# Kernel optimization log

Hardware: AMD Instinct MI355X
Metric: run time of the kernel (lower is better)

## Reference

```python
import jax, jax.numpy as jnp
import numpy as np

SDIM, VDIM, HID, DEPTH = 128, 3, 64, 4
N, E = 50000, 800000
CUTOFF = 5.0


def setup_inputs() -> dict:
    key = jax.random.key(0)
    ks = jax.random.split(key, 16)
    s = jax.random.normal(ks[0], (N, SDIM), jnp.float32)
    v = jax.random.normal(ks[1], (N, 3, VDIM), jnp.float32)
    edge_index = jax.random.randint(ks[2], (2, E), 0, N, dtype=jnp.int32).astype(jnp.int64)
    d = jax.random.uniform(ks[3], (E,), jnp.float32) * CUTOFF
    r = jax.random.normal(ks[4], (E, 3), jnp.float32)
    r = r / jnp.linalg.norm(r, axis=-1, keepdims=True)
    batch = jnp.zeros((N,), jnp.int64)

    def w(k, shape):
        return jax.random.normal(k, shape, jnp.float32) / jnp.sqrt(jnp.float32(shape[-2]))

    return {
        's': s, 'v': v, 'edge_index': edge_index, 'd': d, 'r': r, 'batch': batch,
        'We1': w(ks[5], (DEPTH, 2 * SDIM + 1, HID)), 'be1': jnp.zeros((DEPTH, HID), jnp.float32),
        'We2': w(ks[6], (DEPTH, HID, HID)), 'be2': jnp.zeros((DEPTH, HID), jnp.float32),
        'Wn1': w(ks[7], (DEPTH, SDIM + HID, HID)), 'bn1': jnp.zeros((DEPTH, HID), jnp.float32),
        'Wn2': w(ks[8], (DEPTH, HID, SDIM)), 'bn2': jnp.zeros((DEPTH, SDIM), jnp.float32),
        'Wv': w(ks[9], (DEPTH, HID, 2 * VDIM)), 'bv': jnp.zeros((DEPTH, 2 * VDIM), jnp.float32),
    }


def _egcl(s, v, src, dst, d, r, C, deg, We1, be1, We2, be2, Wn1, bn1, Wn2, bn2, Wv, bv):
    n = s.shape[0]
    # edge message MLP on gathered endpoint features + distance
    x = jnp.concatenate([s[dst], s[src], d[:, None]], axis=-1)   # [E, 2*SDIM+1]
    h = jax.nn.silu(x @ We1 + be1)
    h = jax.nn.silu(h @ We2 + be2)
    h = h * C[:, None]                                            # cutoff envelope
    # scalar update
    agg_s = jax.ops.segment_sum(h, dst, num_segments=n)           # [N, HID]
    u = jax.nn.silu(jnp.concatenate([s, agg_s], axis=-1) @ Wn1 + bn1)
    s = s + (u @ Wn2 + bn2)
    # equivariant vector update: gated neighbor vectors + gated edge directions
    gates = h @ Wv + bv                                           # [E, 2*VDIM]
    g1, g2 = gates[:, :VDIM], gates[:, VDIM:]
    mv = v[src] * g1[:, None, :] + r[:, :, None] * g2[:, None, :] # [E, 3, VDIM]
    agg_v = jax.ops.segment_sum(mv, dst, num_segments=n) / deg[:, None, None]  # mean aggr
    v = v + agg_v
    return s, v


def reference(s, v, edge_index, d, r, batch, We1, be1, We2, be2, Wn1, bn1, Wn2, bn2, Wv, bv):
    src, dst = edge_index[0], edge_index[1]
    C = 0.5 * (jnp.cos(jnp.pi * d / CUTOFF) + 1.0) * (d < CUTOFF).astype(d.dtype)
    deg = jax.ops.segment_sum(jnp.ones_like(d), dst, num_segments=s.shape[0])
    deg = jnp.maximum(deg, 1.0)
    for i in range(DEPTH):
        s, v = _egcl(s, v, src, dst, d, r, C, deg,
                     We1[i], be1[i], We2[i], be2[i],
                     Wn1[i], bn1[i], Wn2[i], bn2[i], Wv[i], bv[i])
    return (s, v)
```

## Files before the change

### kernel.cpp

```cpp
#include <hip/hip_runtime.h>
#include <math.h>

#define SDIM 128
#define HID 64
#define DEPTH 4
#define CUTOFF_F 5.0f
#define CHUNK 4096

typedef __attribute__((ext_vector_type(8))) short bf16x8;
typedef __attribute__((ext_vector_type(4))) float f32x4;
typedef float4 __attribute__((aligned(4))) float4_u;

__device__ __forceinline__ float silu_f(float x) {
    float e = __expf(-x);
    return x * __builtin_amdgcn_rcpf(1.0f + e);
}

__device__ __forceinline__ unsigned short f2bf(float x) {
    __bf16 b = (__bf16)x;
    return __builtin_bit_cast(unsigned short, b);
}
__device__ __forceinline__ unsigned int f2bf2(float a, float b) {
    return (unsigned int)f2bf(a) | ((unsigned int)f2bf(b) << 16);
}
__device__ __forceinline__ float bf2f(unsigned short u) {
    return __uint_as_float(((unsigned int)u) << 16);
}

struct f8 { float v[8]; };
__device__ __forceinline__ f8 load8(const float* p) {
    f8 r;
    float4 a = *(const float4*)p;
    float4 b = *(const float4*)(p + 4);
    r.v[0]=a.x; r.v[1]=a.y; r.v[2]=a.z; r.v[3]=a.w;
    r.v[4]=b.x; r.v[5]=b.y; r.v[6]=b.z; r.v[7]=b.w;
    return r;
}
__device__ __forceinline__ bf16x8 pack8(const float* h) {
    bf16x8 o;
#pragma unroll
    for (int j = 0; j < 8; ++j) o[j] = (short)f2bf(h[j]);
    return o;
}
__device__ __forceinline__ void unpack8(bf16x8 b, float* o) {
#pragma unroll
    for (int j = 0; j < 8; ++j)
        o[j] = __uint_as_float(((unsigned int)(unsigned short)b[j]) << 16);
}

__global__ void detect_idx_kernel(const void* ei, int N, int* flag) {
    int lane = threadIdx.x;
    const long long* p64 = (const long long*)ei;
    long long v = p64[lane];
    bool ok = (v >= 0 && v < (long long)N);
    unsigned long long m = __ballot(ok);
    if (lane == 0) *flag = (m == ~0ull) ? 1 : 0;
}

__global__ void decode_idx_kernel(const void* ei, int E, int N, const int* flag,
                                  int* __restrict__ srcw, int* __restrict__ dstw,
                                  int* __restrict__ deg_i) {
    int i = blockIdx.x * blockDim.x + threadIdx.x;
    if (i >= 2 * E) return;
    int v;
    if (*flag) v = (int)((const long long*)ei)[i];
    else       v = ((const int*)ei)[i];
    v = min(max(v, 0), N - 1);
    if (i < E) {
        srcw[i] = v;
    } else {
        dstw[i - E] = v;
        atomicAdd(&deg_i[v], 1);
    }
}

__global__ __launch_bounds__(256) void scan1_kernel(const int* __restrict__ deg_i,
                                                    int* __restrict__ part, int N) {
    __shared__ int wsum[4];
    int b = blockIdx.x, t = threadIdx.x;
    int base = b * CHUNK;
    int sum = 0;
    for (int i = t; i < CHUNK; i += 256) {
        int idx = base + i;
        sum += (idx < N) ? deg_i[idx] : 0;
    }
#pragma unroll
    for (int off = 32; off; off >>= 1) sum += __shfl_down(sum, off, 64);
    if ((t & 63) == 0) wsum[t >> 6] = sum;
    __syncthreads();
    if (t == 0) part[b] = wsum[0] + wsum[1] + wsum[2] + wsum[3];
}

__global__ void scan2_kernel(int* __restrict__ part, int* __restrict__ row_start,
                             int B1, int N) {
    int t = threadIdx.x;
    int v = (t < B1) ? part[t] : 0;
    int incl = v;
#pragma unroll
    for (int off = 1; off < 64; off <<= 1) {
        int x = __shfl_up(incl, off, 64);
        if (t >= off) incl += x;
    }
    if (t < B1) part[t] = incl - v;
    if (t == 63) row_start[N] = incl;
}

__global__ __launch_bounds__(256) void scan3_kernel(const int* __restrict__ deg_i,
                                                    const int* __restrict__ part,
                                                    int* __restrict__ row_start, int N) {
    __shared__ int wsum[4];
    __shared__ int carry_s;
    int b = blockIdx.x, t = threadIdx.x;
    int lane = t & 63, w = t >> 6;
    if (t == 0) carry_s = part[b];
    __syncthreads();
    int base0 = b * CHUNK;
    for (int base = base0; base < base0 + CHUNK; base += 256) {
        int i = base + t;
        int v = (i < N) ? deg_i[i] : 0;
        int incl = v;
#pragma unroll
        for (int off = 1; off < 64; off <<= 1) {
            int x = __shfl_up(incl, off, 64);
            if (lane >= off) incl += x;
        }
        if (lane == 63) wsum[w] = incl;
        __syncthreads();
        int wpre = 0;
#pragma unroll
        for (int k = 0; k < 4; ++k) if (k < w) wpre += wsum[k];
        int total = wsum[0] + wsum[1] + wsum[2] + wsum[3];
        int carry = carry_s;
        if (i < N) row_start[i] = carry + wpre + incl - v;
        __syncthreads();
        if (t == 0) carry_s = carry + total;
        __syncthreads();
    }
}

__global__ void scatter_kernel(const int* __restrict__ srcw, const int* __restrict__ dstw,
                               const float* __restrict__ dvec, const float* __restrict__ rvec,
                               const int* __restrict__ row_start, int* __restrict__ cursor,
                               float* __restrict__ rec, int E) {
    int e = blockIdx.x * blockDim.x + threadIdx.x;
    if (e >= E) return;
    int dd = dstw[e];
    int ofs = atomicAdd(&cursor[dd], 1);
    int pos = row_start[dd] + ofs;
    float dv = dvec[e];
    float c = 0.5f * (cosf(3.14159265358979323846f * dv * (1.0f / CUTOFF_F)) + 1.0f);
    c = (dv < CUTOFF_F) ? c : 0.0f;
    float4 r0 = make_float4(__int_as_float(srcw[e]), __int_as_float(dd), dv, c);
    float4 r1 = make_float4(rvec[(size_t)e * 3 + 0], rvec[(size_t)e * 3 + 1],
                            rvec[(size_t)e * 3 + 2], 0.0f);
    *(float4*)(rec + (size_t)pos * 8)     = r0;
    *(float4*)(rec + (size_t)pos * 8 + 4) = r1;
}

__global__ __launch_bounds__(256) void wprep_kernel(
    const float* __restrict__ We1, const float* __restrict__ We2,
    const float* __restrict__ Wv,  const float* __restrict__ Wn1,
    const float* __restrict__ Wn2,
    unsigned short* __restrict__ We1t, unsigned short* __restrict__ We2t,
    unsigned short* __restrict__ Wvt,  unsigned short* __restrict__ Wn1t,
    unsigned short* __restrict__ Wn2t) {
    int l = blockIdx.x, t = threadIdx.x;
    const float* W2 = We2 + (size_t)l * HID * HID;
    unsigned short* T2 = We2t + (size_t)l * HID * HID;
    for (int idx = t; idx < HID * HID; idx += 256) {
        int n = idx >> 6, k = idx & 63;
        T2[n * 64 + k] = f2bf(W2[k * HID + n]);
    }
    const float* Wvl = Wv + (size_t)l * HID * 6;
    unsigned short* Tv = Wvt + (size_t)l * 16 * 64;
    for (int idx = t; idx < 16 * 64; idx += 256) {
        int n = idx >> 6, k = idx & 63;
        Tv[idx] = (n < 6) ? f2bf(Wvl[k * 6 + n]) : (unsigned short)0;
    }
    const float* W1 = We1 + (size_t)l * 257 * 64;
    unsigned short* T1 = We1t + (size_t)l * 128 * 128;
    for (int idx = t; idx < 128 * 128; idx += 256) {
        int n = idx >> 7, k = idx & 127;
        float w = (n < 64) ? W1[(size_t)k * 64 + n] : W1[(size_t)(k + 128) * 64 + (n - 64)];
        T1[n * 128 + k] = f2bf(w);
    }
    const float* Wn1l = Wn1 + (size_t)l * 192 * 64;
    unsigned short* Tn1 = Wn1t + (size_t)l * 64 * 192;
    for (int idx = t; idx < 64 * 192; idx += 256) {
        int n = idx / 192, k = idx - n * 192;
        Tn1[idx] = f2bf(Wn1l[(size_t)k * 64 + n]);
    }
    const float* Wn2l = Wn2 + (size_t)l * 64 * 128;
    unsigned short* Tn2 = Wn2t + (size_t)l * 128 * 64;
    for (int idx = t; idx < 128 * 64; idx += 256) {
        int n = idx >> 6, k = idx & 63;
        Tn2[idx] = f2bf(Wn2l[(size_t)k * 128 + n]);
    }
}

__global__ __launch_bounds__(128) void node_pre_kernel(
    const float* __restrict__ s, const unsigned short* __restrict__ We1t,
    const float* __restrict__ be1,
    unsigned short* __restrict__ Pa, unsigned short* __restrict__ Pb, int N)
{
    __shared__ unsigned short sa[16 * 136];
    int t = threadIdx.x;
    int lane = t & 63, w = t >> 6;
    int n0 = blockIdx.x * 16;
    for (int idx = t; idx < 512; idx += 128) {
        int rl = idx >> 5, c4 = (idx & 31) << 2;
        int n = n0 + rl;
        float4 val = make_float4(0.f, 0.f, 0.f, 0.f);
        if (n < N) val = *(const float4*)(s + (size_t)n * SDIM + c4);
        *(uint2*)(sa + rl * 136 + c4) = make_uint2(f2bf2(val.x, val.y), f2bf2(val.z, val.w));
    }
    __syncthreads();
    int lm = lane & 15, lq = lane >> 4;
    int nr = n0 + lm;
    bool rowok = (nr < N);

    bf16x8 af[4];
#pragma unroll
    for (int kc = 0; kc < 4; ++kc)
        af[kc] = *(const bf16x8*)(sa + lm * 136 + kc * 32 + lq * 8);

#pragma unroll
    for (int ct2 = 0; ct2 < 4; ++ct2) {
        int ct = w * 4 + ct2;
        f32x4 acc = {0.f, 0.f, 0.f, 0.f};
#pragma unroll
        for (int kc = 0; kc < 4; ++kc) {
            bf16x8 b = *(const bf16x8*)(We1t + (size_t)(ct * 16 + lm) * 128 + kc * 32 + lq * 8);
            acc = __builtin_amdgcn_mfma_f32_16x16x32_bf16(b, af[kc], acc, 0, 0, 0);
        }
        if (rowok) {
            if (ct < 4) {
                float4 b4 = *(const float4*)(be1 + ct * 16 + lq * 4);
                *(uint2*)(Pa + (size_t)nr * HID + ct * 16 + lq * 4) =
                    make_uint2(f2bf2(acc[0] + b4.x, acc[1] + b4.y),
                               f2bf2(acc[2] + b4.z, acc[3] + b4.w));
            } else {
                *(uint2*)(Pb + (size_t)nr * HID + (ct - 4) * 16 + lq * 4) =
                    make_uint2(f2bf2(acc[0], acc[1]), f2bf2(acc[2], acc[3]));
            }
        }
    }
}

__global__ __launch_bounds__(256) void edge_kernel(
    const float* __restrict__ rec,
    const unsigned short* __restrict__ Pa, const unsigned short* __restrict__ Pb,
    const float* __restrict__ wd,
    const unsigned short* __restrict__ We2t, const float* __restrict__ be2,
    const unsigned short* __restrict__ Wvt, const float* __restrict__ bv,
    const float* __restrict__ v,
    float* __restrict__ agg_s, float* __restrict__ agg_v, int E)
{
    __shared__ unsigned short hb[64 * 72];
    __shared__ float  gl[64 * 8];
    __shared__ float  vb[64 * 12];
    __shared__ int    m_dst[64];
    __shared__ float4 m_r4[64];
    int t = threadIdx.x;
    int e0 = blockIdx.x * 64;
    int lane = t & 63, w = t >> 6;
    int lm = lane & 15, lq = lane >> 4;
    int m0 = w * 16, rm = m0 + lm;
    int ka = lq * 8, kb = 32 + lq * 8;

    int e  = e0 + rm;
    int ec = min(e, E - 1);
    float4 r0 = *(const float4*)(rec + (size_t)ec * 8);
    int srcr = __float_as_int(r0.x);
    int dstr = __float_as_int(r0.y);
    float dv = r0.z;
    float Cr = (e < E) ? r0.w : 0.0f;

    const unsigned short* pa = Pa + (size_t)dstr * HID;
    const unsigned short* pb = Pb + (size_t)srcr * HID;
    bf16x8 ba0 = *(const bf16x8*)(pa + ka);
    bf16x8 bb0 = *(const bf16x8*)(pb + ka);
    bf16x8 ba1 = *(const bf16x8*)(pa + kb);
    bf16x8 bb1 = *(const bf16x8*)(pb + kb);
    f8 xw = load8(wd + ka), yw = load8(wd + kb);

    if (lq == 0) {
        m_dst[rm] = dstr;
        m_r4[rm]  = *(const float4*)(rec + (size_t)ec * 8 + 4);
    }
    {
        const float* vr = v + (size_t)srcr * 9;
        if (lq < 2) {
            float4_u a = *(const float4_u*)(vr + lq * 4);
            *(float4*)(vb + rm * 12 + lq * 4) = make_float4(a.x, a.y, a.z, a.w);
        } else if (lq == 2) {
            vb[rm * 12 + 8] = vr[8];
        }
    }
    bf16x8 wv0 = *(const bf16x8*)(Wvt + (size_t)lm * 64 + ka);
    bf16x8 wv1 = *(const bf16x8*)(Wvt + (size_t)lm * 64 + kb);

    bf16x8 afr0, afr1;
    {
        float fa[8], fb[8], h1[8];
        unpack8(ba0, fa); unpack8(bb0, fb);
#pragma unroll
        for (int j = 0; j < 8; ++j) h1[j] = silu_f(fa[j] + fb[j] + dv * xw.v[j]);
        afr0 = pack8(h1);
        unpack8(ba1, fa); unpack8(bb1, fb);
#pragma unroll
        for (int j = 0; j < 8; ++j) h1[j] = silu_f(fa[j] + fb[j] + dv * yw.v[j]);
        afr1 = pack8(h1);
    }

#pragma unroll
    for (int t4 = 0; t4 < 4; ++t4) {
        bf16x8 a0 = *(const bf16x8*)(We2t + (size_t)(t4 * 16 + lm) * 64 + ka);
        bf16x8 a1 = *(const bf16x8*)(We2t + (size_t)(t4 * 16 + lm) * 64 + kb);
        f32x4 a = {0.f, 0.f, 0.f, 0.f};
        a = __builtin_amdgcn_mfma_f32_16x16x32_bf16(a0, afr0, a, 0, 0, 0);
        a = __builtin_amdgcn_mfma_f32_16x16x32_bf16(a1, afr1, a, 0, 0, 0);
        float4 b4 = *(const float4*)(be2 + t4 * 16 + lq * 4);
        unsigned int p0 = f2bf2(silu_f(a[0] + b4.x) * Cr, silu_f(a[1] + b4.y) * Cr);
        unsigned int p1 = f2bf2(silu_f(a[2] + b4.z) * Cr, silu_f(a[3] + b4.w) * Cr);
        *(uint2*)(hb + rm * 72 + t4 * 16 + lq * 4) = make_uint2(p0, p1);
    }
    __builtin_amdgcn_wave_barrier();

    {
        bf16x8 hb0 = *(const bf16x8*)(hb + rm * 72 + ka);
        bf16x8 hb1 = *(const bf16x8*)(hb + rm * 72 + kb);
        f32x4 ga = {0.f, 0.f, 0.f, 0.f};
        ga = __builtin_amdgcn_mfma_f32_16x16x32_bf16(wv0, hb0, ga, 0, 0, 0);
        ga = __builtin_amdgcn_mfma_f32_16x16x32_bf16(wv1, hb1, ga, 0, 0, 0);
        int er2 = m0 + lm;
        if (lq == 0) {
            float4_u bb = *(const float4_u*)bv;
            *(float4*)(gl + er2 * 8) =
                make_float4(ga[0] + bb.x, ga[1] + bb.y, ga[2] + bb.z, ga[3] + bb.w);
        } else if (lq == 1) {
            gl[er2 * 8 + 4] = ga[0] + bv[4];
            gl[er2 * 8 + 5] = ga[1] + bv[5];
        }
    }

    {
        int c = lane;
        float acc = 0.f;
        int cur = m_dst[m0];
#pragma unroll 4
        for (int r = m0; r < m0 + 16; ++r) {
            int dr = m_dst[r];
            if (dr != cur) {
                atomicAdd(&agg_s[(size_t)cur * HID + c], acc);
                acc = 0.f; cur = dr;
            }
            acc += bf2f(hb[r * 72 + c]);
        }
        atomicAdd(&agg_s[(size_t)cur * HID + c], acc);
    }
    __builtin_amdgcn_wave_barrier();

    if (lane < 36) {
        int seg = lane / 9;
        int c = lane - seg * 9;
        int i = c / 3, j = c - i * 3;
        int r0v = m0 + seg * 4;
        const float* mrf = (const float*)m_r4;
        float acc = 0.f;
        int cur = m_dst[r0v];
#pragma unroll
        for (int r = 0; r < 4; ++r) {
            int rr = r0v + r;
            int dr = m_dst[rr];
            if (dr != cur) {
                atomicAdd(&agg_v[(size_t)cur * 9 + c], acc);
                acc = 0.f; cur = dr;
            }
            if (e0 + rr < E) {
                acc += vb[rr * 12 + c] * gl[rr * 8 + j]
                     + mrf[rr * 4 + i] * gl[rr * 8 + 3 + j];
            }
        }
        atomicAdd(&agg_v[(size_t)cur * 9 + c], acc);
    }
}

__global__ __launch_bounds__(128) void node_fused_kernel(
    float* __restrict__ s, float* __restrict__ vout,
    float* __restrict__ agg_s, float* __restrict__ agg_v,
    const int* __restrict__ row_start,
    const unsigned short* __restrict__ Wn1t, const float* __restrict__ bn1,
    const unsigned short* __restrict__ Wn2t, const float* __restrict__ bn2,
    const unsigned short* __restrict__ We1tn, const float* __restrict__ be1n,
    unsigned short* __restrict__ Pa, unsigned short* __restrict__ Pb,
    int N, int do_pre)
{
    __shared__ unsigned short xa[16 * 200];
    __shared__ unsigned short ub[16 * 72];
    int t = threadIdx.x;
    int lane = t & 63, w = t >> 6;
    int n0 = blockIdx.x * 16;

    for (int idx = t; idx < 144; idx += 128) {
        int rl = idx / 9, c = idx - rl * 9;
        int n2 = n0 + rl;
        if (n2 < N) {
            float av = agg_v[(size_t)n2 * 9 + c];
            agg_v[(size_t)n2 * 9 + c] = 0.f;
            float dg = fmaxf((float)(row_start[n2 + 1] - row_start[n2]), 1.0f);
            vout[(size_t)n2 * 9 + c] += av / dg;
        }
    }

    for (int idx = t; idx < 512; idx += 128) {
        int rl = idx >> 5, c4 = (idx & 31) << 2;
        int n = n0 + rl;
        float4 val = make_float4(0.f, 0.f, 0.f, 0.f);
        if (n < N) val = *(const float4*)(s + (size_t)n * SDIM + c4);
        *(uint2*)(xa + rl * 200 + c4) = make_uint2(f2bf2(val.x, val.y), f2bf2(val.z, val.w));
    }
    for (int idx = t; idx < 256; idx += 128) {
        int rl = idx >> 4, c4 = (idx & 15) << 2;
        int n = n0 + rl;
        float4 val = make_float4(0.f, 0.f, 0.f, 0.f);
        if (n < N) {
            float* ap = agg_s + (size_t)n * HID + c4;
            val = *(const float4*)ap;
            *(float4*)ap = make_float4(0.f, 0.f, 0.f, 0.f);
        }
        *(uint2*)(xa + rl * 200 + 128 + c4) = make_uint2(f2bf2(val.x, val.y), f2bf2(val.z, val.w));
    }
    __syncthreads();

    int lm = lane & 15, lq = lane >> 4;
    int nr = n0 + lm;
    bool rowok = (nr < N);

    bf16x8 af[6];
#pragma unroll
    for (int kc = 0; kc < 6; ++kc)
        af[kc] = *(const bf16x8*)(xa + lm * 200 + kc * 32 + lq * 8);

#pragma unroll
    for (int ct2 = 0; ct2 < 2; ++ct2) {
        int ct = w * 2 + ct2;
        f32x4 acc = {0.f, 0.f, 0.f, 0.f};
#pragma unroll
        for (int kc = 0; kc < 6; ++kc) {
            bf16x8 b = *(const bf16x8*)(Wn1t + (size_t)(ct * 16 + lm) * 192 + kc * 32 + lq * 8);
            acc = __builtin_amdgcn_mfma_f32_16x16x32_bf16(b, af[kc], acc, 0, 0, 0);
        }
        float4 b4 = *(const float4*)(bn1 + ct * 16 + lq * 4);
        unsigned int p0 = f2bf2(silu_f(acc[0] + b4.x), silu_f(acc[1] + b4.y));
        unsigned int p1 = f2bf2(silu_f(acc[2] + b4.z), silu_f(acc[3] + b4.w));
        *(uint2*)(ub + lm * 72 + ct * 16 + lq * 4) = make_uint2(p0, p1);
    }
    __syncthreads();

    unsigned short* sa = xa;
    bf16x8 uf[2];
#pragma unroll
    for (int kc = 0; kc < 2; ++kc)
        uf[kc] = *(const bf16x8*)(ub + lm * 72 + kc * 32 + lq * 8);

    float4 sld[4];
#pragma unroll
    for (int ct2 = 0; ct2 < 4; ++ct2) {
        int ct = w * 4 + ct2;
        sld[ct2] = rowok ? *(const float4*)(s + (size_t)nr * SDIM + ct * 16 + lq * 4)
                         : make_float4(0.f, 0.f, 0.f, 0.f);
    }

#pragma unroll
    for (int ct2 = 0; ct2 < 4; ++ct2) {
        int ct = w * 4 + ct2;
        f32x4 acc = {0.f, 0.f, 0.f, 0.f};
#pragma unroll
        for (int kc = 0; kc < 2; ++kc) {
            bf16x8 b = *(const bf16x8*)(Wn2t + (size_t)(ct * 16 + lm) * 64 + kc * 32 + lq * 8);
            acc = __builtin_amdgcn_mfma_f32_16x16x32_bf16(b, uf[kc], acc, 0, 0, 0);
        }
        float4 b4 = *(const float4*)(bn2 + ct * 16 + lq * 4);
        if (rowok) {
            float4 sv = make_float4(sld[ct2].x + acc[0] + b4.x,
                                    sld[ct2].y + acc[1] + b4.y,
                                    sld[ct2].z + acc[2] + b4.z,
                                    sld[ct2].w + acc[3] + b4.w);
            *(float4*)(s + (size_t)nr * SDIM + ct * 16 + lq * 4) = sv;
            *(uint2*)(sa + lm * 136 + ct * 16 + lq * 4) =
                make_uint2(f2bf2(sv.x, sv.y), f2bf2(sv.z, sv.w));
        } else {
            *(uint2*)(sa + lm * 136 + ct * 16 + lq * 4) = make_uint2(0u, 0u);
        }
    }
    __syncthreads();

    if (do_pre) {
        bf16x8 pf[4];
#pragma unroll
        for (int kc = 0; kc < 4; ++kc)
            pf[kc] = *(const bf16x8*)(sa + lm * 136 + kc * 32 + lq * 8);

#pragma unroll
        for (int ct2 = 0; ct2 < 4; ++ct2) {
            int ct = w * 4 + ct2;
            f32x4 acc = {0.f, 0.f, 0.f, 0.f};
#pragma unroll
            for (int kc = 0; kc < 4; ++kc) {
                bf16x8 b = *(const bf16x8*)(We1tn + (size_t)(ct * 16 + lm) * 128 + kc * 32 + lq * 8);
                acc = __builtin_amdgcn_mfma_f32_16x16x32_bf16(b, pf[kc], acc, 0, 0, 0);
            }
            if (rowok) {
                if (ct < 4) {
                    float4 b4 = *(const float4*)(be1n + ct * 16 + lq * 4);
                    *(uint2*)(Pa + (size_t)nr * HID + ct * 16 + lq * 4) =
                        make_uint2(f2bf2(acc[0] + b4.x, acc[1] + b4.y),
                                   f2bf2(acc[2] + b4.z, acc[3] + b4.w));
                } else {
                    *(uint2*)(Pb + (size_t)nr * HID + (ct - 4) * 16 + lq * 4) =
                        make_uint2(f2bf2(acc[0], acc[1]), f2bf2(acc[2], acc[3]));
                }
            }
        }
    }
}

extern "C" void kernel_launch(void* const* d_in, const int* in_sizes, int n_in,
                              void* d_out, int out_size, void* d_ws, size_t ws_size,
                              hipStream_t stream)
{
    const float* s_in  = (const float*)d_in[0];
    const float* v_in  = (const float*)d_in[1];
    const void*  ei    = d_in[2];
    const float* d_vec = (const float*)d_in[3];
    const float* r_vec = (const float*)d_in[4];
    const float* We1 = (const float*)d_in[6];
    const float* be1 = (const float*)d_in[7];
    const float* We2 = (const float*)d_in[8];
    const float* be2 = (const float*)d_in[9];
    const float* Wn1 = (const float*)d_in[10];
    const float* bn1 = (const float*)d_in[11];
    const float* Wn2 = (const float*)d_in[12];
    const float* bn2 = (const float*)d_in[13];
    const float* Wv  = (const float*)d_in[14];
    const float* bv  = (const float*)d_in[15];

    int N = in_sizes[0] / SDIM;
    int E = in_sizes[3];

    float* out_s = (float*)d_out;
    float* out_v = out_s + (size_t)N * SDIM;

    char* wp = (char*)d_ws;
    auto alloc = [&wp](size_t bytes) -> char* {
        char* p = wp;
        wp += (bytes + 31) & ~(size_t)31;
        return p;
    };
    float* rec       = (float*)alloc((size_t)E * 8 * 4);
    unsigned short* Pa = (unsigned short*)alloc((size_t)N * HID * 2);
    unsigned short* Pb = (unsigned short*)alloc((size_t)N * HID * 2);
    float* agg_s     = (float*)alloc((size_t)N * HID * 4);
    float* agg_v     = (float*)alloc((size_t)N * 9 * 4);
    int*   deg_i     = (int*)alloc((size_t)N * 4);
    int*   cursor    = (int*)alloc((size_t)N * 4);
    int*   row_start = (int*)alloc((size_t)(N + 1) * 4);
    int*   part      = (int*)alloc(64 * 4);
    int*   flag      = (int*)alloc(16);
    int*   srcw      = (int*)alloc((size_t)E * 4);
    int*   dstw      = (int*)alloc((size_t)E * 4);
    unsigned short* We2t = (unsigned short*)alloc((size_t)DEPTH * HID * HID * 2);
    unsigned short* Wvt  = (unsigned short*)alloc((size_t)DEPTH * 16 * 64 * 2);
    unsigned short* We1t = (unsigned short*)alloc((size_t)DEPTH * 128 * 128 * 2);
    unsigned short* Wn1t = (unsigned short*)alloc((size_t)DEPTH * 64 * 192 * 2);
    unsigned short* Wn2t = (unsigned short*)alloc((size_t)DEPTH * 128 * 64 * 2);

    hipMemcpyAsync(out_s, s_in, (size_t)N * SDIM * sizeof(float),
                   hipMemcpyDeviceToDevice, stream);
    hipMemcpyAsync(out_v, v_in, (size_t)N * 9 * sizeof(float),
                   hipMemcpyDeviceToDevice, stream);

    detect_idx_kernel<<<1, 64, 0, stream>>>(ei, N, flag);
    hipMemsetAsync(deg_i, 0, (size_t)N * 2 * sizeof(int), stream);
    hipMemsetAsync(agg_s, 0, (size_t)N * (HID + 9) * sizeof(float), stream);
    decode_idx_kernel<<<(2 * E + 255) / 256, 256, 0, stream>>>(ei, E, N, flag,
                                                               srcw, dstw, deg_i);
    int B1 = (N + CHUNK - 1) / CHUNK;
    scan1_kernel<<<B1, 256, 0, stream>>>(deg_i, part, N);
    scan2_kernel<<<1, 64, 0, stream>>>(part, row_start, B1, N);
    scan3_kernel<<<B1, 256, 0, stream>>>(deg_i, part, row_start, N);
    scatter_kernel<<<(E + 255) / 256, 256, 0, stream>>>(srcw, dstw, d_vec, r_vec,
                                                        row_start, cursor, rec, E);
    wprep_kernel<<<DEPTH, 256, 0, stream>>>(We1, We2, Wv, Wn1, Wn2,
                                            We1t, We2t, Wvt, Wn1t, Wn2t);

    int nb_n = (N + 15) / 16;
    int nb_e = (E + 63) / 64;
    node_pre_kernel<<<nb_n, 128, 0, stream>>>(out_s, We1t, be1, Pa, Pb, N);
    for (int l = 0; l < DEPTH; ++l) {
        int ln = (l + 1 < DEPTH) ? (l + 1) : 0;
        const float* We1_l = We1 + (size_t)l * 257 * 64;
        const float* be2_l = be2 + (size_t)l * 64;
        const float* bn1_l = bn1 + (size_t)l * 64;
        const float* bn2_l = bn2 + (size_t)l * 128;
        const float* bv_l  = bv  + (size_t)l * 6;
        const float* be1_n = be1 + (size_t)ln * 64;
        const unsigned short* We2t_l = We2t + (size_t)l * HID * HID;
        const unsigned short* Wvt_l  = Wvt  + (size_t)l * 16 * 64;
        const unsigned short* Wn1t_l = Wn1t + (size_t)l * 64 * 192;
        const unsigned short* Wn2t_l = Wn2t + (size_t)l * 128 * 64;
        const unsigned short* We1t_n = We1t + (size_t)ln * 128 * 128;

        edge_kernel<<<nb_e, 256, 0, stream>>>(rec, Pa, Pb,
                                              We1_l + 256 * 64,
                                              We2t_l, be2_l, Wvt_l, bv_l,
                                              out_v, agg_s, agg_v, E);
        node_fused_kernel<<<nb_n, 128, 0, stream>>>(out_s, out_v, agg_s, agg_v,
                                                    row_start,
                                                    Wn1t_l, bn1_l, Wn2t_l, bn2_l,
                                                    We1t_n, be1_n, Pa, Pb,
                                                    N, (l + 1 < DEPTH) ? 1 : 0);
    }
}
```

Measured before the change: 791.4 us.

## Split edge scatter into permutation pass and drop initial output copies

The edge scatter now runs in two passes. The first writes only a permutation index at the atomically reserved CSR position. The second builds the packed edge records in sorted order, so the 32-byte record writes become coalesced instead of scattered. The initial device-to-device copies of s and v into the outputs are removed: layer 0 reads the inputs directly and the node kernel writes out = in + update. This adds one extra kernel launch and a permutation buffer, and makes the gathers of the per-edge inputs random.

Result: slower. 821.4 us (+3.8%).

```diff
diff --git a/kernel.cpp b/kernel.cpp
--- a/kernel.cpp
+++ b/kernel.cpp
@@ -138,19 +138,28 @@
     }
 }
 
-__global__ void scatter_kernel(const int* __restrict__ srcw, const int* __restrict__ dstw,
-                               const float* __restrict__ dvec, const float* __restrict__ rvec,
-                               const int* __restrict__ row_start, int* __restrict__ cursor,
-                               float* __restrict__ rec, int E) {
+__global__ void scatter_perm_kernel(const int* __restrict__ dstw,
+                                    const int* __restrict__ row_start,
+                                    int* __restrict__ cursor,
+                                    int* __restrict__ perm, int E) {
     int e = blockIdx.x * blockDim.x + threadIdx.x;
     if (e >= E) return;
     int dd = dstw[e];
-    int ofs = atomicAdd(&cursor[dd], 1);
-    int pos = row_start[dd] + ofs;
+    int pos = row_start[dd] + atomicAdd(&cursor[dd], 1);
+    perm[pos] = e;
+}
+
+__global__ void rec_build_kernel(const int* __restrict__ perm,
+                                 const int* __restrict__ srcw, const int* __restrict__ dstw,
+                                 const float* __restrict__ dvec, const float* __restrict__ rvec,
+                                 float* __restrict__ rec, int E) {
+    int pos = blockIdx.x * blockDim.x + threadIdx.x;
+    if (pos >= E) return;
+    int e = perm[pos];
     float dv = dvec[e];
     float c = 0.5f * (cosf(3.14159265358979323846f * dv * (1.0f / CUTOFF_F)) + 1.0f);
     c = (dv < CUTOFF_F) ? c : 0.0f;
-    float4 r0 = make_float4(__int_as_float(srcw[e]), __int_as_float(dd), dv, c);
+    float4 r0 = make_float4(__int_as_float(srcw[e]), __int_as_float(dstw[e]), dv, c);
     float4 r1 = make_float4(rvec[(size_t)e * 3 + 0], rvec[(size_t)e * 3 + 1],
                             rvec[(size_t)e * 3 + 2], 0.0f);
     *(float4*)(rec + (size_t)pos * 8)     = r0;
@@ -387,7 +396,8 @@
 }
 
 __global__ __launch_bounds__(128) void node_fused_kernel(
-    float* __restrict__ s, float* __restrict__ vout,
+    const float* __restrict__ s_in_p, float* __restrict__ s_out_p,
+    const float* __restrict__ v_in_p, float* __restrict__ v_out_p,
     float* __restrict__ agg_s, float* __restrict__ agg_v,
     const int* __restrict__ row_start,
     const unsigned short* __restrict__ Wn1t, const float* __restrict__ bn1,
@@ -409,7 +419,7 @@
             float av = agg_v[(size_t)n2 * 9 + c];
             agg_v[(size_t)n2 * 9 + c] = 0.f;
             float dg = fmaxf((float)(row_start[n2 + 1] - row_start[n2]), 1.0f);
-            vout[(size_t)n2 * 9 + c] += av / dg;
+            v_out_p[(size_t)n2 * 9 + c] = v_in_p[(size_t)n2 * 9 + c] + av / dg;
         }
     }
 
@@ -417,7 +427,7 @@
         int rl = idx >> 5, c4 = (idx & 31) << 2;
         int n = n0 + rl;
         float4 val = make_float4(0.f, 0.f, 0.f, 0.f);
-        if (n < N) val = *(const float4*)(s + (size_t)n * SDIM + c4);
+        if (n < N) val = *(const float4*)(s_in_p + (size_t)n * SDIM + c4);
         *(uint2*)(xa + rl * 200 + c4) = make_uint2(f2bf2(val.x, val.y), f2bf2(val.z, val.w));
     }
     for (int idx = t; idx < 256; idx += 128) {
@@ -468,7 +478,7 @@
 #pragma unroll
     for (int ct2 = 0; ct2 < 4; ++ct2) {
         int ct = w * 4 + ct2;
-        sld[ct2] = rowok ? *(const float4*)(s + (size_t)nr * SDIM + ct * 16 + lq * 4)
+        sld[ct2] = rowok ? *(const float4*)(s_in_p + (size_t)nr * SDIM + ct * 16 + lq * 4)
                          : make_float4(0.f, 0.f, 0.f, 0.f);
     }
 
@@ -487,7 +497,7 @@
                                     sld[ct2].y + acc[1] + b4.y,
                                     sld[ct2].z + acc[2] + b4.z,
                                     sld[ct2].w + acc[3] + b4.w);
-            *(float4*)(s + (size_t)nr * SDIM + ct * 16 + lq * 4) = sv;
+            *(float4*)(s_out_p + (size_t)nr * SDIM + ct * 16 + lq * 4) = sv;
             *(uint2*)(sa + lm * 136 + ct * 16 + lq * 4) =
                 make_uint2(f2bf2(sv.x, sv.y), f2bf2(sv.z, sv.w));
         } else {
@@ -570,16 +580,12 @@
     int*   flag      = (int*)alloc(16);
     int*   srcw      = (int*)alloc((size_t)E * 4);
     int*   dstw      = (int*)alloc((size_t)E * 4);
+    int*   perm      = (int*)alloc((size_t)E * 4);
     unsigned short* We2t = (unsigned short*)alloc((size_t)DEPTH * HID * HID * 2);
     unsigned short* Wvt  = (unsigned short*)alloc((size_t)DEPTH * 16 * 64 * 2);
     unsigned short* We1t = (unsigned short*)alloc((size_t)DEPTH * 128 * 128 * 2);
     unsigned short* Wn1t = (unsigned short*)alloc((size_t)DEPTH * 64 * 192 * 2);
     unsigned short* Wn2t = (unsigned short*)alloc((size_t)DEPTH * 128 * 64 * 2);
-
-    hipMemcpyAsync(out_s, s_in, (size_t)N * SDIM * sizeof(float),
-                   hipMemcpyDeviceToDevice, stream);
-    hipMemcpyAsync(out_v, v_in, (size_t)N * 9 * sizeof(float),
-                   hipMemcpyDeviceToDevice, stream);
 
     detect_idx_kernel<<<1, 64, 0, stream>>>(ei, N, flag);
     hipMemsetAsync(deg_i, 0, (size_t)N * 2 * sizeof(int), stream);
@@ -590,14 +596,16 @@
     scan1_kernel<<<B1, 256, 0, stream>>>(deg_i, part, N);
     scan2_kernel<<<1, 64, 0, stream>>>(part, row_start, B1, N);
     scan3_kernel<<<B1, 256, 0, stream>>>(deg_i, part, row_start, N);
-    scatter_kernel<<<(E + 255) / 256, 256, 0, stream>>>(srcw, dstw, d_vec, r_vec,
-                                                        row_start, cursor, rec, E);
+    scatter_perm_kernel<<<(E + 255) / 256, 256, 0, stream>>>(dstw, row_start,
+                                                             cursor, perm, E);
+    rec_build_kernel<<<(E + 255) / 256, 256, 0, stream>>>(perm, srcw, dstw,
+                                                          d_vec, r_vec, rec, E);
     wprep_kernel<<<DEPTH, 256, 0, stream>>>(We1, We2, Wv, Wn1, Wn2,
                                             We1t, We2t, Wvt, Wn1t, Wn2t);
 
     int nb_n = (N + 15) / 16;
     int nb_e = (E + 63) / 64;
-    node_pre_kernel<<<nb_n, 128, 0, stream>>>(out_s, We1t, be1, Pa, Pb, N);
+    node_pre_kernel<<<nb_n, 128, 0, stream>>>(s_in, We1t, be1, Pa, Pb, N);
     for (int l = 0; l < DEPTH; ++l) {
         int ln = (l + 1 < DEPTH) ? (l + 1) : 0;
         const float* We1_l = We1 + (size_t)l * 257 * 64;
@@ -612,12 +620,15 @@
         const unsigned short* Wn2t_l = Wn2t + (size_t)l * 128 * 64;
         const unsigned short* We1t_n = We1t + (size_t)ln * 128 * 128;
 
+        const float* s_rd = (l == 0) ? s_in : out_s;
+        const float* v_rd = (l == 0) ? v_in : out_v;
+
         edge_kernel<<<nb_e, 256, 0, stream>>>(rec, Pa, Pb,
                                               We1_l + 256 * 64,
                                               We2t_l, be2_l, Wvt_l, bv_l,
-                                              out_v, agg_s, agg_v, E);
-        node_fused_kernel<<<nb_n, 128, 0, stream>>>(out_s, out_v, agg_s, agg_v,
-                                                    row_start,
+                                              v_rd, agg_s, agg_v, E);
+        node_fused_kernel<<<nb_n, 128, 0, stream>>>(s_rd, out_s, v_rd, out_v,
+                                                    agg_s, agg_v, row_start,
                                                     Wn1t_l, bn1_l, Wn2t_l, bn2_l,
                                                     We1t_n, be1_n, Pa, Pb,
                                                     N, (l + 1 < DEPTH) ? 1 : 0);
```
